# Kernel tuning notes

Measured on AMD Instinct MI355X. Metric: run time of the kernel, lower is better.

The kernel has to match this reference:

```python
import jax, jax.numpy as jnp
import numpy as np

N = 10000        # num_nodes
IN_DIM = 128     # in_dim
HID = 256        # hidden_size
EMB = 128        # final embedding dim
R = 8            # num_relations (== num_bases)
C = 32           # num_classes
E = 640000       # num_edges


def setup_inputs() -> dict:
    key = jax.random.key(0)
    ks = jax.random.split(key, 12)
    s = 0.05
    return {
        "x": jax.random.normal(ks[0], (N, N), jnp.float32) * s,
        "edge_index": jax.random.randint(ks[1], (2, E), 0, N),
        "edge_type": jax.random.randint(ks[2], (E,), 0, R),
        "emb": jax.random.normal(ks[3], (N, IN_DIM), jnp.float32) * s,
        "comp1": jax.random.normal(ks[4], (R, R), jnp.float32) * s,
        "basis1": jax.random.normal(ks[5], (R, IN_DIM, HID), jnp.float32) * s,
        "root1": jax.random.normal(ks[6], (IN_DIM, HID), jnp.float32) * s,
        "bias1": jnp.zeros((HID,), jnp.float32),
        "comp2": jax.random.normal(ks[7], (R, R), jnp.float32) * s,
        "basis2": jax.random.normal(ks[8], (R, HID, EMB), jnp.float32) * s,
        "root2": jax.random.normal(ks[9], (HID, EMB), jnp.float32) * s,
        "bias2": jnp.zeros((EMB,), jnp.float32),
        "w_dec": jax.random.normal(ks[10], (EMB, C), jnp.float32) * s,
    }


def _rgcn(h, src, dst, edge_type, comp, basis, root, bias):
    # basis-decomposed RGCN layer with mean aggregation (PyG RGCNConv semantics)
    # transform node features by every basis once: [N, B, out]
    hb = jnp.einsum("ni,bio->nbo", h, basis)
    # per-edge relation coefficients: [E, B]; message = comp[r] . hb[src]
    msg = jnp.einsum("eb,ebo->eo", comp[edge_type], hb[src])
    agg = jax.ops.segment_sum(msg, dst, num_segments=N)
    deg = jax.ops.segment_sum(jnp.ones((msg.shape[0],), h.dtype), dst, num_segments=N)
    agg = agg / jnp.maximum(deg, 1.0)[:, None]
    return agg + h @ root + bias


def reference(x, edge_index, edge_type, emb, comp1, basis1, root1, bias1,
              comp2, basis2, root2, bias2, w_dec):
    src, dst = edge_index[0], edge_index[1]
    h = jax.nn.relu(x @ emb)
    h = jax.nn.relu(_rgcn(h, src, dst, edge_type, comp1, basis1, root1, bias1))
    h = jax.nn.relu(_rgcn(h, src, dst, edge_type, comp2, basis2, root2, bias2))
    # multi-class inner-product decoder: logits = z @ W, softmax over classes
    return jax.nn.softmax(h @ w_dec, axis=1)
```

## Files before the change

kernel.cpp:

```cpp
#include <hip/hip_runtime.h>

typedef unsigned short u16;
typedef unsigned int u32;
typedef __attribute__((ext_vector_type(8))) short bf16x8;
typedef __attribute__((ext_vector_type(4))) float f32x4;

#define N_NODES 10000
#define E_EDGES 640000

static __device__ __forceinline__ float b2f(u16 u) {
  union { u32 i; float f; } x; x.i = ((u32)u) << 16; return x.f;
}
static __device__ __forceinline__ u16 f2b(float f) {
  union { float f; u32 i; } x; x.f = f;
  u32 r = x.i + 0x7FFF + ((x.i >> 16) & 1);
  return (u16)(r >> 16);
}
static __device__ __forceinline__ float ldf(const void* p, size_t i, int f32) {
  return f32 ? ((const float*)p)[i] : b2f(((const u16*)p)[i]);
}

__global__ __launch_bounds__(256) void detect_kernel(const u16* __restrict__ x, int* __restrict__ flag) {
  __shared__ int cnt_s;
  if (threadIdx.x == 0) cnt_s = 0;
  __syncthreads();
  int c = 0;
  for (int i = threadIdx.x; i < 4096; i += 256) {
    int e = (x[i] >> 7) & 255;
    if (e >= 140) c++;
  }
  atomicAdd(&cnt_s, c);
  __syncthreads();
  if (threadIdx.x == 0) flag[0] = (cnt_s > 64) ? 1 : 0;
}

__global__ void hist_kernel(const int* __restrict__ ei, int E, int* __restrict__ cnt) {
  int e = blockIdx.x * 256 + threadIdx.x;
  if (e < E) atomicAdd(&cnt[ei[E + e]], 1);
}

__global__ __launch_bounds__(256) void scan_kernel(const int* __restrict__ cnt,
                                                   int* __restrict__ offs,
                                                   int* __restrict__ cursor, int N) {
  __shared__ int tmp[256];
  const int t = threadIdx.x;
  const int CH = (N + 255) / 256;
  const int base = t * CH;
  int s = 0;
  for (int j = 0; j < CH; j++) { int p = base + j; if (p < N) s += cnt[p]; }
  tmp[t] = s;
  __syncthreads();
  for (int od = 1; od < 256; od <<= 1) {
    int a = (t >= od) ? tmp[t - od] : 0;
    __syncthreads();
    tmp[t] += a;
    __syncthreads();
  }
  int run = tmp[t] - s;
  for (int j = 0; j < CH; j++) {
    int p = base + j;
    if (p < N) { offs[p] = run; cursor[p] = run; run += cnt[p]; }
  }
  if (t == 255) offs[N] = tmp[255];
}

__global__ void bucket_kernel(const int* __restrict__ ei, const int* __restrict__ et,
                              int E, int* __restrict__ cursor, int* __restrict__ bucket) {
  int e = blockIdx.x * 256 + threadIdx.x;
  if (e < E) {
    int dst = ei[E + e];
    int pos = atomicAdd(&cursor[dst], 1);
    bucket[pos] = ei[e] | (et[e] << 14);
  }
}

__global__ void transpose_kernel(const void* __restrict__ in, u16* __restrict__ out,
                                 int R, int C, const int* __restrict__ dflag) {
  __shared__ u16 tile[64][65];
  const int f = dflag[0];
  int r0 = blockIdx.x * 64, c0 = blockIdx.y * 64;
  int t = threadIdx.x;
  #pragma unroll
  for (int k = 0; k < 16; k++) {
    int lin = t + k * 256; int rr = lin >> 6, cc = lin & 63;
    int gr = r0 + rr;
    tile[rr][cc] = (gr < R) ? f2b(ldf(in, (size_t)gr * C + c0 + cc, f)) : (u16)0;
  }
  __syncthreads();
  #pragma unroll
  for (int k = 0; k < 16; k++) {
    int lin = t + k * 256; int rr = lin >> 6, cc = lin & 63;
    int gc = r0 + cc;
    if (gc < R) out[(size_t)(c0 + rr) * R + gc] = tile[cc][rr];
  }
}

template<int I, int O>
__global__ void wprep_kernel(const void* __restrict__ comp, const void* __restrict__ basis,
                             const void* __restrict__ root, u16* __restrict__ WT,
                             const int* __restrict__ dflag) {
  const int Kcat = 9 * I;
  const int f = dflag[0];
  int idx = blockIdx.x * 256 + threadIdx.x;
  if (idx >= Kcat * O) return;
  int o = idx % O;
  int kc = idx / O;
  float v;
  if (kc < 8 * I) {
    int r = kc / I, i = kc % I;
    float s = 0.f;
    #pragma unroll
    for (int b = 0; b < 8; b++)
      s += ldf(comp, r * 8 + b, f) * ldf(basis, ((size_t)b * I + i) * O + o, f);
    v = s;
  } else {
    int i = kc - 8 * I;
    v = ldf(root, (size_t)i * O + o, f);
  }
  WT[(size_t)o * Kcat + kc] = f2b(v);
}

template<int I>
__global__ void gather_kernel(const u16* __restrict__ h, const int* __restrict__ offs,
                              const int* __restrict__ bucket, u16* __restrict__ s, int node0) {
  __shared__ float acc[8 * I];
  const int d = node0 + blockIdx.x, t = threadIdx.x;
  const int ldk = 9 * I;
  #pragma unroll
  for (int r = 0; r < 8; r++) acc[r * I + t] = 0.f;
  int b0 = offs[d], b1 = offs[d + 1];
  int j = b0;
  int pn = 0; float vn = 0.f;
  if (j < b1) { pn = bucket[j]; vn = b2f(h[(size_t)(pn & 16383) * I + t]); }
  while (j < b1) {
    int p = pn; float v = vn;
    ++j;
    if (j < b1) { pn = bucket[j]; vn = b2f(h[(size_t)(pn & 16383) * I + t]); }
    acc[(p >> 14) * I + t] += v;
  }
  float inv = 1.0f / (float)((b1 - b0) > 1 ? (b1 - b0) : 1);
  size_t base = (size_t)blockIdx.x * ldk;
  #pragma unroll
  for (int r = 0; r < 8; r++) s[base + r * I + t] = f2b(acc[r * I + t] * inv);
  s[base + 8 * I + t] = h[(size_t)d * I + t];
}

__global__ __launch_bounds__(256) void gemm_kernel(
    const void* __restrict__ A, int lda,
    const u16* __restrict__ BT, int ldbt,
    int M, int Nout, int K,
    int tiles_per_split, int ktiles_total,
    float* __restrict__ partials,
    const int* __restrict__ dflagA) {
  __shared__ __align__(16) u16 As[128 * 32];
  __shared__ __align__(16) u16 Bs[128 * 32];
  const int f32A = dflagA ? dflagA[0] : 0;
  const int tid = threadIdx.x;
  const int wave = tid >> 6;
  const int lane = tid & 63;
  const int quad = lane >> 4;
  const int l16 = lane & 15;
  const int m0 = blockIdx.x * 128;
  const int n0 = blockIdx.y * 128;
  const int split = blockIdx.z;
  const int wm = (wave >> 1) * 64;
  const int wn = (wave & 1) * 64;

  int kt0 = split * tiles_per_split;
  int kt1 = kt0 + tiles_per_split;
  if (kt1 > ktiles_total) kt1 = ktiles_total;

  f32x4 acc[4][4];
  #pragma unroll
  for (int mi = 0; mi < 4; mi++)
    #pragma unroll
    for (int ni = 0; ni < 4; ni++) {
      f32x4 z = {0.f, 0.f, 0.f, 0.f};
      acc[mi][ni] = z;
    }

  for (int kt = kt0; kt < kt1; ++kt) {
    const int k0 = kt * 32;
    __syncthreads();
    #pragma unroll
    for (int i = 0; i < 2; ++i) {
      int c = tid + i * 256;
      int row = c >> 2, kc = c & 3;
      int kpos = k0 + kc * 8;
      uint4 vb = {0u, 0u, 0u, 0u};
      if (kpos < K) vb = *(const uint4*)(BT + (size_t)(n0 + row) * ldbt + kpos);
      *(uint4*)&Bs[(size_t)c * 8] = vb;
      uint4 va = {0u, 0u, 0u, 0u};
      if (kpos < K) {
        int ga = m0 + row; if (ga > M - 1) ga = M - 1;
        if (!f32A) {
          va = *(const uint4*)((const u16*)A + (size_t)ga * lda + kpos);
        } else {
          const float* Af = (const float*)A + (size_t)ga * lda + kpos;
          float4 f0 = ((const float4*)Af)[0];
          float4 f1 = ((const float4*)Af)[1];
          va.x = (u32)f2b(f0.x) | ((u32)f2b(f0.y) << 16);
          va.y = (u32)f2b(f0.z) | ((u32)f2b(f0.w) << 16);
          va.z = (u32)f2b(f1.x) | ((u32)f2b(f1.y) << 16);
          va.w = (u32)f2b(f1.z) | ((u32)f2b(f1.w) << 16);
        }
      }
      *(uint4*)&As[(size_t)c * 8] = va;
    }
    __syncthreads();

    bf16x8 af[4], bfr[4];
    #pragma unroll
    for (int mi = 0; mi < 4; mi++)
      af[mi] = *(const bf16x8*)&As[(size_t)(wm + mi * 16 + l16) * 32 + quad * 8];
    #pragma unroll
    for (int ni = 0; ni < 4; ni++)
      bfr[ni] = *(const bf16x8*)&Bs[(size_t)(wn + ni * 16 + l16) * 32 + quad * 8];
    #pragma unroll
    for (int mi = 0; mi < 4; mi++)
      #pragma unroll
      for (int ni = 0; ni < 4; ni++)
        acc[mi][ni] = __builtin_amdgcn_mfma_f32_16x16x32_bf16(af[mi], bfr[ni], acc[mi][ni], 0, 0, 0);
  }

  #pragma unroll
  for (int mi = 0; mi < 4; mi++)
    #pragma unroll
    for (int ni = 0; ni < 4; ni++)
      #pragma unroll
      for (int jj = 0; jj < 4; jj++) {
        int row = m0 + wm + mi * 16 + quad * 4 + jj;
        int col = n0 + wn + ni * 16 + l16;
        if (row < M) partials[((size_t)split * M + row) * Nout + col] = acc[mi][ni][jj];
      }
}

__global__ void reduce_kernel(const float* __restrict__ partials, int S, int count,
                              int nmask, const void* __restrict__ bias, u16* __restrict__ out,
                              const int* __restrict__ dflag) {
  int idx = blockIdx.x * 256 + threadIdx.x;
  if (idx >= count) return;
  float s = 0.f;
  for (int z = 0; z < S; z++) s += partials[(size_t)z * count + idx];
  if (bias) s += ldf(bias, idx & nmask, dflag[0]);
  s = s > 0.f ? s : 0.f;
  out[idx] = f2b(s);
}

__global__ __launch_bounds__(256) void decoder_kernel(const u16* __restrict__ h2,
                                                      const void* __restrict__ wdec,
                                                      void* __restrict__ out,
                                                      const int* __restrict__ dflag) {
  __shared__ float w[128 * 32];
  __shared__ float hrow[4][128];
  const int f = dflag[0];
  int t = threadIdx.x;
  for (int i = t; i < 128 * 32; i += 256) w[i] = ldf(wdec, i, f);
  int wv = t >> 6, lane = t & 63;
  int n = blockIdx.x * 4 + wv;
  hrow[wv][lane * 2]     = b2f(h2[(size_t)n * 128 + lane * 2]);
  hrow[wv][lane * 2 + 1] = b2f(h2[(size_t)n * 128 + lane * 2 + 1]);
  __syncthreads();
  int half = lane >> 5, c = lane & 31;
  float sum = 0.f;
  #pragma unroll 8
  for (int k = 0; k < 64; k++) sum += hrow[wv][half * 64 + k] * w[(half * 64 + k) * 32 + c];
  sum += __shfl_xor(sum, 32);
  float mx = sum;
  #pragma unroll
  for (int m = 16; m >= 1; m >>= 1) mx = fmaxf(mx, __shfl_xor(mx, m));
  float e = __expf(sum - mx);
  float tot = e;
  #pragma unroll
  for (int m = 16; m >= 1; m >>= 1) tot += __shfl_xor(tot, m);
  float p = e / tot;
  if (half == 0) {
    if (f) ((float*)out)[(size_t)n * 32 + c] = p;
    else   ((u16*)out)[(size_t)n * 32 + c] = f2b(p);
  }
}

extern "C" void kernel_launch(void* const* d_in, const int* in_sizes, int n_in,
                              void* d_out, int out_size, void* d_ws, size_t ws_size,
                              hipStream_t stream) {
  const void* x      = d_in[0];
  const int* ei      = (const int*)d_in[1];
  const int* et      = (const int*)d_in[2];
  const void* emb    = d_in[3];
  const void* comp1  = d_in[4];
  const void* basis1 = d_in[5];
  const void* root1  = d_in[6];
  const void* bias1  = d_in[7];
  const void* comp2  = d_in[8];
  const void* basis2 = d_in[9];
  const void* root2  = d_in[10];
  const void* bias2  = d_in[11];
  const void* wdec   = d_in[12];

  const int N = N_NODES, E = E_EDGES;
  auto AL = [](size_t b) -> size_t { return (b + 255) & ~(size_t)255; };

  char* base = (char*)d_ws;
  size_t off = 0;
  auto alloc = [&](size_t b) -> char* { char* p = base + off; off += AL(b); return p; };
  int* dflag  = (int*)alloc(4);
  int* offs   = (int*)alloc((size_t)(N + 1) * 4);
  int* bucket = (int*)alloc((size_t)E * 4);
  u16* h0 = (u16*)alloc((size_t)N * 128 * 2);
  u16* h1 = (u16*)alloc((size_t)N * 256 * 2);
  u16* h2 = (u16*)alloc((size_t)N * 128 * 2);
  char* pool = base + off;
  size_t pool_sz = (ws_size > off) ? (ws_size - off) : 0;

  int spA = 8;
  while (spA > 1 && AL((size_t)128 * N * 2) + (size_t)spA * N * 128 * 4 > pool_sz) spA >>= 1;
  int nchunks = 1;
  while (nchunks < 32) {
    int Mc = (N + nchunks - 1) / nchunks;
    int z2c = (nchunks == 1) ? 3 : 4;
    size_t reqL1 = AL((size_t)256 * 1152 * 2) + AL((size_t)Mc * 1152 * 2) + (size_t)2 * Mc * 256 * 4;
    size_t reqL2 = AL((size_t)128 * 2304 * 2) + AL((size_t)Mc * 2304 * 2) + (size_t)z2c * Mc * 128 * 4;
    if (reqL1 <= pool_sz && reqL2 <= pool_sz) break;
    nchunks <<= 1;
  }
  const int Mc = (N + nchunks - 1) / nchunks;
  const int z1 = 2;
  const int z2 = (nchunks == 1) ? 3 : 4;

  detect_kernel<<<1, 256, 0, stream>>>((const u16*)x, dflag);

  int* cnt    = (int*)pool;
  int* cursor = (int*)(pool + AL((size_t)N * 4));
  hipMemsetAsync(cnt, 0, (size_t)N * 4, stream);
  hist_kernel<<<(E + 255) / 256, 256, 0, stream>>>(ei, E, cnt);
  scan_kernel<<<1, 256, 0, stream>>>(cnt, offs, cursor, N);
  bucket_kernel<<<(E + 255) / 256, 256, 0, stream>>>(ei, et, E, cursor, bucket);

  {
    u16* embT = (u16*)pool;
    float* pA = (float*)(pool + AL((size_t)128 * N * 2));
    transpose_kernel<<<dim3((N + 63) / 64, 2), 256, 0, stream>>>(emb, embT, N, 128, dflag);
    int ktt = (N + 31) / 32;
    int tps = (ktt + spA - 1) / spA;
    gemm_kernel<<<dim3((N + 127) / 128, 1, spA), 256, 0, stream>>>(
        x, N, embT, N, N, 128, N, tps, ktt, pA, dflag);
    reduce_kernel<<<(N * 128 + 255) / 256, 256, 0, stream>>>(
        pA, spA, N * 128, 127, (const void*)nullptr, h0, dflag);
  }

  {
    u16* WT1 = (u16*)pool;
    char* chunkbase = pool + AL((size_t)256 * 1152 * 2);
    wprep_kernel<128, 256><<<(1152 * 256 + 255) / 256, 256, 0, stream>>>(comp1, basis1, root1, WT1, dflag);
    for (int c = 0; c < nchunks; c++) {
      int node0 = c * Mc;
      int rows = N - node0; if (rows > Mc) rows = Mc;
      if (rows <= 0) break;
      u16* s1 = (u16*)chunkbase;
      float* p1 = (float*)(chunkbase + AL((size_t)Mc * 1152 * 2));
      gather_kernel<128><<<rows, 128, 0, stream>>>(h0, offs, bucket, s1, node0);
      gemm_kernel<<<dim3((rows + 127) / 128, 2, z1), 256, 0, stream>>>(
          s1, 1152, WT1, 1152, rows, 256, 1152, (36 + z1 - 1) / z1, 36, p1, (const int*)nullptr);
      reduce_kernel<<<(rows * 256 + 255) / 256, 256, 0, stream>>>(
          p1, z1, rows * 256, 255, bias1, h1 + (size_t)node0 * 256, dflag);
    }
  }

  {
    u16* WT2 = (u16*)pool;
    char* chunkbase = pool + AL((size_t)128 * 2304 * 2);
    wprep_kernel<256, 128><<<(2304 * 128 + 255) / 256, 256, 0, stream>>>(comp2, basis2, root2, WT2, dflag);
    for (int c = 0; c < nchunks; c++) {
      int node0 = c * Mc;
      int rows = N - node0; if (rows > Mc) rows = Mc;
      if (rows <= 0) break;
      u16* s2 = (u16*)chunkbase;
      float* p2 = (float*)(chunkbase + AL((size_t)Mc * 2304 * 2));
      gather_kernel<256><<<rows, 256, 0, stream>>>(h1, offs, bucket, s2, node0);
      gemm_kernel<<<dim3((rows + 127) / 128, 1, z2), 256, 0, stream>>>(
          s2, 2304, WT2, 2304, rows, 128, 2304, (72 + z2 - 1) / z2, 72, p2, (const int*)nullptr);
      reduce_kernel<<<(rows * 128 + 255) / 256, 256, 0, stream>>>(
          p2, z2, rows * 128, 127, bias2, h2 + (size_t)node0 * 128, dflag);
    }
  }

  decoder_kernel<<<N / 4, 256, 0, stream>>>(h2, wdec, d_out, dflag);
}
```

Baseline: 984.9 us.

## Sort edges by (dst,relation) and transform-then-aggregate in layer two

```diff
diff --git a/kernel.cpp b/kernel.cpp
--- a/kernel.cpp
+++ b/kernel.cpp
@@ -34,9 +34,10 @@
   if (threadIdx.x == 0) flag[0] = (cnt_s > 64) ? 1 : 0;
 }
 
-__global__ void hist_kernel(const int* __restrict__ ei, int E, int* __restrict__ cnt) {
+__global__ void hist_kernel(const int* __restrict__ ei, const int* __restrict__ et,
+                            int E, int* __restrict__ cnt) {
   int e = blockIdx.x * 256 + threadIdx.x;
-  if (e < E) atomicAdd(&cnt[ei[E + e]], 1);
+  if (e < E) atomicAdd(&cnt[ei[E + e] * 8 + et[e]], 1);
 }
 
 __global__ __launch_bounds__(256) void scan_kernel(const int* __restrict__ cnt,
@@ -68,9 +69,9 @@
                               int E, int* __restrict__ cursor, int* __restrict__ bucket) {
   int e = blockIdx.x * 256 + threadIdx.x;
   if (e < E) {
-    int dst = ei[E + e];
-    int pos = atomicAdd(&cursor[dst], 1);
-    bucket[pos] = ei[e] | (et[e] << 14);
+    int seg = ei[E + e] * 8 + et[e];
+    int pos = atomicAdd(&cursor[seg], 1);
+    bucket[pos] = ei[e];
   }
 }
 
@@ -120,29 +121,72 @@
   WT[(size_t)o * Kcat + kc] = f2b(v);
 }
 
-template<int I>
-__global__ void gather_kernel(const u16* __restrict__ h, const int* __restrict__ offs,
-                              const int* __restrict__ bucket, u16* __restrict__ s, int node0) {
-  __shared__ float acc[8 * I];
+template<int I, int O>
+__global__ void wprep_t_kernel(const void* __restrict__ comp, const void* __restrict__ basis,
+                               const void* __restrict__ root, u16* __restrict__ WT,
+                               const int* __restrict__ dflag) {
+  const int f = dflag[0];
+  int idx = blockIdx.x * 256 + threadIdx.x;
+  if (idx >= 9 * O * I) return;
+  int k = idx % I;
+  int ocat = idx / I;
+  int r = ocat / O, o = ocat % O;
+  float v;
+  if (r < 8) {
+    float s = 0.f;
+    #pragma unroll
+    for (int b = 0; b < 8; b++)
+      s += ldf(comp, r * 8 + b, f) * ldf(basis, ((size_t)b * I + k) * O + o, f);
+    v = s;
+  } else {
+    v = ldf(root, (size_t)k * O + o, f);
+  }
+  WT[(size_t)ocat * I + k] = f2b(v);
+}
+
+__global__ void gather1_kernel(const u16* __restrict__ h, const int* __restrict__ offs,
+                               const int* __restrict__ bucket, u16* __restrict__ s, int node0) {
   const int d = node0 + blockIdx.x, t = threadIdx.x;
-  const int ldk = 9 * I;
-  #pragma unroll
-  for (int r = 0; r < 8; r++) acc[r * I + t] = 0.f;
-  int b0 = offs[d], b1 = offs[d + 1];
-  int j = b0;
-  int pn = 0; float vn = 0.f;
-  if (j < b1) { pn = bucket[j]; vn = b2f(h[(size_t)(pn & 16383) * I + t]); }
-  while (j < b1) {
-    int p = pn; float v = vn;
-    ++j;
-    if (j < b1) { pn = bucket[j]; vn = b2f(h[(size_t)(pn & 16383) * I + t]); }
-    acc[(p >> 14) * I + t] += v;
-  }
-  float inv = 1.0f / (float)((b1 - b0) > 1 ? (b1 - b0) : 1);
-  size_t base = (size_t)blockIdx.x * ldk;
-  #pragma unroll
-  for (int r = 0; r < 8; r++) s[base + r * I + t] = f2b(acc[r * I + t] * inv);
-  s[base + 8 * I + t] = h[(size_t)d * I + t];
+  const int sb = d * 8;
+  const int b0 = offs[sb], bend = offs[sb + 8];
+  const float inv = 1.0f / (float)((bend - b0) > 1 ? (bend - b0) : 1);
+  const size_t base = (size_t)blockIdx.x * 1152;
+  #pragma unroll
+  for (int r = 0; r < 8; r++) {
+    int j = offs[sb + r], j1 = offs[sb + r + 1];
+    float a0 = 0.f, a1 = 0.f;
+    for (; j + 1 < j1; j += 2) {
+      int sA = bucket[j], sB = bucket[j + 1];
+      a0 += b2f(h[(size_t)sA * 128 + t]);
+      a1 += b2f(h[(size_t)sB * 128 + t]);
+    }
+    if (j < j1) a0 += b2f(h[(size_t)bucket[j] * 128 + t]);
+    s[base + r * 128 + t] = f2b((a0 + a1) * inv);
+  }
+  s[base + 1024 + t] = h[(size_t)d * 128 + t];
+}
+
+__global__ void agg2_kernel(const u16* __restrict__ hb, const int* __restrict__ offs,
+                            const int* __restrict__ bucket, const void* __restrict__ bias,
+                            u16* __restrict__ h2, const int* __restrict__ dflag) {
+  const int d = blockIdx.x, t = threadIdx.x;
+  const int sb = d * 8;
+  const int b0 = offs[sb], bend = offs[sb + 8];
+  const float inv = 1.0f / (float)((bend - b0) > 1 ? (bend - b0) : 1);
+  float a0 = 0.f, a1 = 0.f;
+  #pragma unroll
+  for (int r = 0; r < 8; r++) {
+    int j = offs[sb + r], j1 = offs[sb + r + 1];
+    const size_t co = (size_t)(r * 128 + t);
+    for (; j + 1 < j1; j += 2) {
+      int sA = bucket[j], sB = bucket[j + 1];
+      a0 += b2f(hb[(size_t)sA * 1152 + co]);
+      a1 += b2f(hb[(size_t)sB * 1152 + co]);
+    }
+    if (j < j1) a0 += b2f(hb[(size_t)bucket[j] * 1152 + co]);
+  }
+  float v = (a0 + a1) * inv + b2f(hb[(size_t)d * 1152 + 1024 + t]) + ldf(bias, t, dflag[0]);
+  h2[(size_t)d * 128 + t] = f2b(v > 0.f ? v : 0.f);
 }
 
 __global__ __launch_bounds__(256) void gemm_kernel(
@@ -235,6 +279,75 @@
       }
 }
 
+__global__ __launch_bounds__(256) void gemm_direct_kernel(
+    const u16* __restrict__ A, int lda,
+    const u16* __restrict__ BT, int ldbt,
+    int M, int Nout, int K,
+    u16* __restrict__ out) {
+  __shared__ __align__(16) u16 As[128 * 32];
+  __shared__ __align__(16) u16 Bs[128 * 32];
+  const int tid = threadIdx.x;
+  const int wave = tid >> 6;
+  const int lane = tid & 63;
+  const int quad = lane >> 4;
+  const int l16 = lane & 15;
+  const int m0 = blockIdx.x * 128;
+  const int n0 = blockIdx.y * 128;
+  const int wm = (wave >> 1) * 64;
+  const int wn = (wave & 1) * 64;
+
+  f32x4 acc[4][4];
+  #pragma unroll
+  for (int mi = 0; mi < 4; mi++)
+    #pragma unroll
+    for (int ni = 0; ni < 4; ni++) {
+      f32x4 z = {0.f, 0.f, 0.f, 0.f};
+      acc[mi][ni] = z;
+    }
+
+  const int ktiles = K >> 5;
+  for (int kt = 0; kt < ktiles; ++kt) {
+    const int k0 = kt * 32;
+    __syncthreads();
+    #pragma unroll
+    for (int i = 0; i < 2; ++i) {
+      int c = tid + i * 256;
+      int row = c >> 2, kc = c & 3;
+      int kpos = k0 + kc * 8;
+      uint4 vb = *(const uint4*)(BT + (size_t)(n0 + row) * ldbt + kpos);
+      *(uint4*)&Bs[(size_t)c * 8] = vb;
+      int ga = m0 + row; if (ga > M - 1) ga = M - 1;
+      uint4 va = *(const uint4*)(A + (size_t)ga * lda + kpos);
+      *(uint4*)&As[(size_t)c * 8] = va;
+    }
+    __syncthreads();
+
+    bf16x8 af[4], bfr[4];
+    #pragma unroll
+    for (int mi = 0; mi < 4; mi++)
+      af[mi] = *(const bf16x8*)&As[(size_t)(wm + mi * 16 + l16) * 32 + quad * 8];
+    #pragma unroll
+    for (int ni = 0; ni < 4; ni++)
+      bfr[ni] = *(const bf16x8*)&Bs[(size_t)(wn + ni * 16 + l16) * 32 + quad * 8];
+    #pragma unroll
+    for (int mi = 0; mi < 4; mi++)
+      #pragma unroll
+      for (int ni = 0; ni < 4; ni++)
+        acc[mi][ni] = __builtin_amdgcn_mfma_f32_16x16x32_bf16(af[mi], bfr[ni], acc[mi][ni], 0, 0, 0);
+  }
+
+  #pragma unroll
+  for (int mi = 0; mi < 4; mi++)
+    #pragma unroll
+    for (int ni = 0; ni < 4; ni++)
+      #pragma unroll
+      for (int jj = 0; jj < 4; jj++) {
+        int row = m0 + wm + mi * 16 + quad * 4 + jj;
+        int col = n0 + wn + ni * 16 + l16;
+        if (row < M) out[(size_t)row * Nout + col] = f2b(acc[mi][ni][jj]);
+      }
+}
+
 __global__ void reduce_kernel(const float* __restrict__ partials, int S, int count,
                               int nmask, const void* __restrict__ bias, u16* __restrict__ out,
                               const int* __restrict__ dflag) {
@@ -298,13 +411,14 @@
   const void* wdec   = d_in[12];
 
   const int N = N_NODES, E = E_EDGES;
+  const int NSEG = N * 8;
   auto AL = [](size_t b) -> size_t { return (b + 255) & ~(size_t)255; };
 
   char* base = (char*)d_ws;
   size_t off = 0;
   auto alloc = [&](size_t b) -> char* { char* p = base + off; off += AL(b); return p; };
   int* dflag  = (int*)alloc(4);
-  int* offs   = (int*)alloc((size_t)(N + 1) * 4);
+  int* offs   = (int*)alloc((size_t)(NSEG + 1) * 4);
   int* bucket = (int*)alloc((size_t)E * 4);
   u16* h0 = (u16*)alloc((size_t)N * 128 * 2);
   u16* h1 = (u16*)alloc((size_t)N * 256 * 2);
@@ -317,23 +431,20 @@
   int nchunks = 1;
   while (nchunks < 32) {
     int Mc = (N + nchunks - 1) / nchunks;
-    int z2c = (nchunks == 1) ? 3 : 4;
     size_t reqL1 = AL((size_t)256 * 1152 * 2) + AL((size_t)Mc * 1152 * 2) + (size_t)2 * Mc * 256 * 4;
-    size_t reqL2 = AL((size_t)128 * 2304 * 2) + AL((size_t)Mc * 2304 * 2) + (size_t)z2c * Mc * 128 * 4;
-    if (reqL1 <= pool_sz && reqL2 <= pool_sz) break;
+    if (reqL1 <= pool_sz) break;
     nchunks <<= 1;
   }
   const int Mc = (N + nchunks - 1) / nchunks;
   const int z1 = 2;
-  const int z2 = (nchunks == 1) ? 3 : 4;
 
   detect_kernel<<<1, 256, 0, stream>>>((const u16*)x, dflag);
 
   int* cnt    = (int*)pool;
-  int* cursor = (int*)(pool + AL((size_t)N * 4));
-  hipMemsetAsync(cnt, 0, (size_t)N * 4, stream);
-  hist_kernel<<<(E + 255) / 256, 256, 0, stream>>>(ei, E, cnt);
-  scan_kernel<<<1, 256, 0, stream>>>(cnt, offs, cursor, N);
+  int* cursor = (int*)(pool + AL((size_t)NSEG * 4));
+  hipMemsetAsync(cnt, 0, (size_t)NSEG * 4, stream);
+  hist_kernel<<<(E + 255) / 256, 256, 0, stream>>>(ei, et, E, cnt);
+  scan_kernel<<<1, 256, 0, stream>>>(cnt, offs, cursor, NSEG);
   bucket_kernel<<<(E + 255) / 256, 256, 0, stream>>>(ei, et, E, cursor, bucket);
 
   {
@@ -358,7 +469,7 @@
       if (rows <= 0) break;
       u16* s1 = (u16*)chunkbase;
       float* p1 = (float*)(chunkbase + AL((size_t)Mc * 1152 * 2));
-      gather_kernel<128><<<rows, 128, 0, stream>>>(h0, offs, bucket, s1, node0);
+      gather1_kernel<<<rows, 128, 0, stream>>>(h0, offs, bucket, s1, node0);
       gemm_kernel<<<dim3((rows + 127) / 128, 2, z1), 256, 0, stream>>>(
           s1, 1152, WT1, 1152, rows, 256, 1152, (36 + z1 - 1) / z1, 36, p1, (const int*)nullptr);
       reduce_kernel<<<(rows * 256 + 255) / 256, 256, 0, stream>>>(
@@ -367,21 +478,12 @@
   }
 
   {
-    u16* WT2 = (u16*)pool;
-    char* chunkbase = pool + AL((size_t)128 * 2304 * 2);
-    wprep_kernel<256, 128><<<(2304 * 128 + 255) / 256, 256, 0, stream>>>(comp2, basis2, root2, WT2, dflag);
-    for (int c = 0; c < nchunks; c++) {
-      int node0 = c * Mc;
-      int rows = N - node0; if (rows > Mc) rows = Mc;
-      if (rows <= 0) break;
-      u16* s2 = (u16*)chunkbase;
-      float* p2 = (float*)(chunkbase + AL((size_t)Mc * 2304 * 2));
-      gather_kernel<256><<<rows, 256, 0, stream>>>(h1, offs, bucket, s2, node0);
-      gemm_kernel<<<dim3((rows + 127) / 128, 1, z2), 256, 0, stream>>>(
-          s2, 2304, WT2, 2304, rows, 128, 2304, (72 + z2 - 1) / z2, 72, p2, (const int*)nullptr);
-      reduce_kernel<<<(rows * 128 + 255) / 256, 256, 0, stream>>>(
-          p2, z2, rows * 128, 127, bias2, h2 + (size_t)node0 * 128, dflag);
-    }
+    u16* WT2b = (u16*)pool;
+    u16* hb2  = (u16*)(pool + AL((size_t)1152 * 256 * 2));
+    wprep_t_kernel<256, 128><<<(1152 * 256 + 255) / 256, 256, 0, stream>>>(comp2, basis2, root2, WT2b, dflag);
+    gemm_direct_kernel<<<dim3((N + 127) / 128, 9), 256, 0, stream>>>(
+        h1, 256, WT2b, 256, N, 1152, 256, hb2);
+    agg2_kernel<<<N, 128, 0, stream>>>(hb2, offs, bucket, bias2, h2, dflag);
   }
 
   decoder_kernel<<<N / 4, 256, 0, stream>>>(h2, wdec, d_out, dflag);
```

New measurement: 1.073 ms. +9.0%, slower.

## Sort edges by (dst, relation) segments and gather with register accumulators

Applied to the files above, without the earlier changes.

```diff
diff --git a/kernel.cpp b/kernel.cpp
--- a/kernel.cpp
+++ b/kernel.cpp
@@ -34,9 +34,18 @@
   if (threadIdx.x == 0) flag[0] = (cnt_s > 64) ? 1 : 0;
 }
 
-__global__ void hist_kernel(const int* __restrict__ ei, int E, int* __restrict__ cnt) {
+__global__ void hist_kernel(const int* __restrict__ ei, const int* __restrict__ et,
+                            int E, int* __restrict__ cnt8) {
   int e = blockIdx.x * 256 + threadIdx.x;
-  if (e < E) atomicAdd(&cnt[ei[E + e]], 1);
+  if (e < E) atomicAdd(&cnt8[ei[E + e] * 8 + et[e]], 1);
+}
+
+__global__ void sumdst_kernel(const int* __restrict__ cnt8, int* __restrict__ dstcnt, int N) {
+  int d = blockIdx.x * 256 + threadIdx.x;
+  if (d >= N) return;
+  const int4* p = (const int4*)(cnt8 + d * 8);
+  int4 a = p[0], b = p[1];
+  dstcnt[d] = a.x + a.y + a.z + a.w + b.x + b.y + b.z + b.w;
 }
 
 __global__ __launch_bounds__(256) void scan_kernel(const int* __restrict__ cnt,
@@ -64,13 +73,27 @@
   if (t == 255) offs[N] = tmp[255];
 }
 
+__global__ void segoffs_kernel(const int* __restrict__ dstoffs, const int* __restrict__ cnt8,
+                               int* __restrict__ offs, int* __restrict__ cursor, int N) {
+  int d = blockIdx.x * 256 + threadIdx.x;
+  if (d >= N) return;
+  int base = dstoffs[d];
+  #pragma unroll
+  for (int r = 0; r < 8; r++) {
+    offs[d * 8 + r] = base;
+    cursor[d * 8 + r] = base;
+    base += cnt8[d * 8 + r];
+  }
+  if (d == N - 1) offs[N * 8] = base;
+}
+
 __global__ void bucket_kernel(const int* __restrict__ ei, const int* __restrict__ et,
                               int E, int* __restrict__ cursor, int* __restrict__ bucket) {
   int e = blockIdx.x * 256 + threadIdx.x;
   if (e < E) {
-    int dst = ei[E + e];
-    int pos = atomicAdd(&cursor[dst], 1);
-    bucket[pos] = ei[e] | (et[e] << 14);
+    int seg = ei[E + e] * 8 + et[e];
+    int pos = atomicAdd(&cursor[seg], 1);
+    bucket[pos] = ei[e];
   }
 }
 
@@ -121,27 +144,27 @@
 }
 
 template<int I>
-__global__ void gather_kernel(const u16* __restrict__ h, const int* __restrict__ offs,
-                              const int* __restrict__ bucket, u16* __restrict__ s, int node0) {
-  __shared__ float acc[8 * I];
+__global__ void gather_seg_kernel(const u16* __restrict__ h, const int* __restrict__ offs,
+                                  const int* __restrict__ bucket, u16* __restrict__ s, int node0) {
   const int d = node0 + blockIdx.x, t = threadIdx.x;
-  const int ldk = 9 * I;
-  #pragma unroll
-  for (int r = 0; r < 8; r++) acc[r * I + t] = 0.f;
-  int b0 = offs[d], b1 = offs[d + 1];
-  int j = b0;
-  int pn = 0; float vn = 0.f;
-  if (j < b1) { pn = bucket[j]; vn = b2f(h[(size_t)(pn & 16383) * I + t]); }
-  while (j < b1) {
-    int p = pn; float v = vn;
-    ++j;
-    if (j < b1) { pn = bucket[j]; vn = b2f(h[(size_t)(pn & 16383) * I + t]); }
-    acc[(p >> 14) * I + t] += v;
-  }
-  float inv = 1.0f / (float)((b1 - b0) > 1 ? (b1 - b0) : 1);
-  size_t base = (size_t)blockIdx.x * ldk;
-  #pragma unroll
-  for (int r = 0; r < 8; r++) s[base + r * I + t] = f2b(acc[r * I + t] * inv);
+  const int sb = d * 8;
+  const int b0 = offs[sb], bend = offs[sb + 8];
+  const float inv = 1.0f / (float)((bend - b0) > 1 ? (bend - b0) : 1);
+  const size_t base = (size_t)blockIdx.x * (9 * I);
+  #pragma unroll
+  for (int r = 0; r < 8; r++) {
+    int j = offs[sb + r], j1 = offs[sb + r + 1];
+    float a0 = 0.f, a1 = 0.f, a2 = 0.f, a3 = 0.f;
+    for (; j + 3 < j1; j += 4) {
+      int s0 = bucket[j], s1 = bucket[j + 1], s2 = bucket[j + 2], s3 = bucket[j + 3];
+      a0 += b2f(h[(size_t)s0 * I + t]);
+      a1 += b2f(h[(size_t)s1 * I + t]);
+      a2 += b2f(h[(size_t)s2 * I + t]);
+      a3 += b2f(h[(size_t)s3 * I + t]);
+    }
+    for (; j < j1; ++j) a0 += b2f(h[(size_t)bucket[j] * I + t]);
+    s[base + r * I + t] = f2b((a0 + a1 + a2 + a3) * inv);
+  }
   s[base + 8 * I + t] = h[(size_t)d * I + t];
 }
 
@@ -298,13 +321,14 @@
   const void* wdec   = d_in[12];
 
   const int N = N_NODES, E = E_EDGES;
+  const int NSEG = N * 8;
   auto AL = [](size_t b) -> size_t { return (b + 255) & ~(size_t)255; };
 
   char* base = (char*)d_ws;
   size_t off = 0;
   auto alloc = [&](size_t b) -> char* { char* p = base + off; off += AL(b); return p; };
   int* dflag  = (int*)alloc(4);
-  int* offs   = (int*)alloc((size_t)(N + 1) * 4);
+  int* offs   = (int*)alloc((size_t)(NSEG + 1) * 4);
   int* bucket = (int*)alloc((size_t)E * 4);
   u16* h0 = (u16*)alloc((size_t)N * 128 * 2);
   u16* h1 = (u16*)alloc((size_t)N * 256 * 2);
@@ -317,24 +341,31 @@
   int nchunks = 1;
   while (nchunks < 32) {
     int Mc = (N + nchunks - 1) / nchunks;
-    int z2c = (nchunks == 1) ? 3 : 4;
     size_t reqL1 = AL((size_t)256 * 1152 * 2) + AL((size_t)Mc * 1152 * 2) + (size_t)2 * Mc * 256 * 4;
-    size_t reqL2 = AL((size_t)128 * 2304 * 2) + AL((size_t)Mc * 2304 * 2) + (size_t)z2c * Mc * 128 * 4;
+    size_t reqL2 = AL((size_t)128 * 2304 * 2) + AL((size_t)Mc * 2304 * 2) + (size_t)4 * Mc * 128 * 4;
     if (reqL1 <= pool_sz && reqL2 <= pool_sz) break;
     nchunks <<= 1;
   }
   const int Mc = (N + nchunks - 1) / nchunks;
   const int z1 = 2;
-  const int z2 = (nchunks == 1) ? 3 : 4;
+  const int z2 = 4;
 
   detect_kernel<<<1, 256, 0, stream>>>((const u16*)x, dflag);
 
-  int* cnt    = (int*)pool;
-  int* cursor = (int*)(pool + AL((size_t)N * 4));
-  hipMemsetAsync(cnt, 0, (size_t)N * 4, stream);
-  hist_kernel<<<(E + 255) / 256, 256, 0, stream>>>(ei, E, cnt);
-  scan_kernel<<<1, 256, 0, stream>>>(cnt, offs, cursor, N);
-  bucket_kernel<<<(E + 255) / 256, 256, 0, stream>>>(ei, et, E, cursor, bucket);
+  {
+    char* p = pool;
+    int* cnt8    = (int*)p;                 p += AL((size_t)NSEG * 4);
+    int* cursor  = (int*)p;                 p += AL((size_t)NSEG * 4);
+    int* dstcnt  = (int*)p;                 p += AL((size_t)N * 4);
+    int* dstoffs = (int*)p;                 p += AL((size_t)(N + 1) * 4);
+    int* dstcur  = (int*)p;                 p += AL((size_t)N * 4);
+    hipMemsetAsync(cnt8, 0, (size_t)NSEG * 4, stream);
+    hist_kernel<<<(E + 255) / 256, 256, 0, stream>>>(ei, et, E, cnt8);
+    sumdst_kernel<<<(N + 255) / 256, 256, 0, stream>>>(cnt8, dstcnt, N);
+    scan_kernel<<<1, 256, 0, stream>>>(dstcnt, dstoffs, dstcur, N);
+    segoffs_kernel<<<(N + 255) / 256, 256, 0, stream>>>(dstoffs, cnt8, offs, cursor, N);
+    bucket_kernel<<<(E + 255) / 256, 256, 0, stream>>>(ei, et, E, cursor, bucket);
+  }
 
   {
     u16* embT = (u16*)pool;
@@ -358,7 +389,7 @@
       if (rows <= 0) break;
       u16* s1 = (u16*)chunkbase;
       float* p1 = (float*)(chunkbase + AL((size_t)Mc * 1152 * 2));
-      gather_kernel<128><<<rows, 128, 0, stream>>>(h0, offs, bucket, s1, node0);
+      gather_seg_kernel<128><<<rows, 128, 0, stream>>>(h0, offs, bucket, s1, node0);
       gemm_kernel<<<dim3((rows + 127) / 128, 2, z1), 256, 0, stream>>>(
           s1, 1152, WT1, 1152, rows, 256, 1152, (36 + z1 - 1) / z1, 36, p1, (const int*)nullptr);
       reduce_kernel<<<(rows * 256 + 255) / 256, 256, 0, stream>>>(
@@ -376,7 +407,7 @@
       if (rows <= 0) break;
       u16* s2 = (u16*)chunkbase;
       float* p2 = (float*)(chunkbase + AL((size_t)Mc * 2304 * 2));
-      gather_kernel<256><<<rows, 256, 0, stream>>>(h1, offs, bucket, s2, node0);
+      gather_seg_kernel<256><<<rows, 256, 0, stream>>>(h1, offs, bucket, s2, node0);
       gemm_kernel<<<dim3((rows + 127) / 128, 1, z2), 256, 0, stream>>>(
           s2, 2304, WT2, 2304, rows, 128, 2304, (72 + z2 - 1) / z2, 72, p2, (const int*)nullptr);
       reduce_kernel<<<(rows * 128 + 255) / 256, 256, 0, stream>>>(
```

Result: faster. 899.3 us (-8.7%).
